# Kernel optimization log

Measured on AMD Instinct MI355X. Metric: run time of the kernel, lower is better.

Reference implementation:

```python
import jax, jax.numpy as jnp
import numpy as np

ROUTING_ITER = 3
EPS = 1e-8


def squash(caps, axis=-1, eps=EPS):
    dot = jnp.sum(caps * caps, axis=axis, keepdims=True)
    scale = dot / (1.0 + dot) / jnp.sqrt(dot + eps)
    return scale * caps


def setup_inputs() -> dict:
    key = jax.random.key(0)
    k1, k2, k3 = jax.random.split(key, 3)
    B, I, O, D_in, D_out = 32, 1024, 64, 16, 32
    x = jax.random.normal(k1, (B, I, D_in), dtype=jnp.float32)
    W = jax.random.normal(k2, (1, I, O, D_out, D_in), dtype=jnp.float32) * 0.05
    b = jax.random.normal(k3, (1, 1, O, D_out), dtype=jnp.float32) * 0.05
    return {"x": x, "W": W, "b": b}


def reference(x, W, b):
    # u_hat[b,i,o,d] = sum_n W[0,i,o,d,n] * x[b,i,n]
    u_hat = jnp.einsum('iodn,bin->biod', W[0], x)  # [B, I, O, D_out]
    u_hat_det = jax.lax.stop_gradient(u_hat)
    B, I, O, _ = u_hat.shape
    b_ij = jnp.zeros((B, I, O, 1), dtype=x.dtype)
    v_j = None
    for it in range(ROUTING_ITER):
        c_ij = jax.nn.softmax(b_ij, axis=2)  # over output capsules
        if it == ROUTING_ITER - 1:
            s_j = jnp.sum(c_ij * u_hat, axis=1, keepdims=True) + b  # [B,1,O,D]
            v_j = squash(s_j, axis=-1)
        else:
            s_j = jnp.sum(c_ij * u_hat_det, axis=1, keepdims=True)
            v_j = squash(s_j, axis=-1)
            a_ij = jnp.sum(u_hat_det * v_j, axis=-1, keepdims=True)  # agreement
            b_ij = b_ij + a_ij
    return jnp.squeeze(v_j)  # [B, O, D_out]
```

## Files before the change

kernel.cpp:

```cpp
#include <hip/hip_runtime.h>
#include <hip/hip_bf16.h>
#include <stdint.h>

#define B_  32
#define I_  1024
#define O_  64
#define D_  32
#define N_  16
#define OD_ 2048

__device__ __forceinline__ uint32_t f2bf1(float f) {
  uint32_t u = __float_as_uint(f);
  return (u + 0x7fffu + ((u >> 16) & 1u)) >> 16;
}
__device__ __forceinline__ uint32_t pack2(float a, float b) {
  return f2bf1(a) | (f2bf1(b) << 16);
}
__device__ __forceinline__ void unpack8(uint4 r, float u[8]) {
  u[0] = __uint_as_float(r.x << 16);
  u[1] = __uint_as_float(r.x & 0xffff0000u);
  u[2] = __uint_as_float(r.y << 16);
  u[3] = __uint_as_float(r.y & 0xffff0000u);
  u[4] = __uint_as_float(r.z << 16);
  u[5] = __uint_as_float(r.z & 0xffff0000u);
  u[6] = __uint_as_float(r.w << 16);
  u[7] = __uint_as_float(r.w & 0xffff0000u);
}

__global__ __launch_bounds__(256) void k_einsum(const float* __restrict__ x,
                                                const float* __restrict__ W,
                                                uint4* __restrict__ uhat) {
  const int i = blockIdx.x;
  const int t = threadIdx.x;
  __shared__ float xs[B_ * N_];
  for (int e = t; e < B_ * N_; e += 256) {
    int bb = e >> 4, n = e & 15;
    xs[e] = x[(size_t)bb * (I_ * N_) + (size_t)i * N_ + n];
  }
  float w[8][16];
  const float* Wi = W + (size_t)i * (OD_ * N_) + (size_t)t * (8 * N_);
  #pragma unroll
  for (int k = 0; k < 8; ++k) {
    #pragma unroll
    for (int q = 0; q < 4; ++q) {
      float4 f = ((const float4*)(Wi + k * 16))[q];
      w[k][q * 4 + 0] = f.x; w[k][q * 4 + 1] = f.y;
      w[k][q * 4 + 2] = f.z; w[k][q * 4 + 3] = f.w;
    }
  }
  __syncthreads();
  for (int bb = 0; bb < B_; ++bb) {
    float xv[16];
    #pragma unroll
    for (int q = 0; q < 4; ++q) {
      float4 f = ((const float4*)(xs + bb * 16))[q];
      xv[q * 4 + 0] = f.x; xv[q * 4 + 1] = f.y;
      xv[q * 4 + 2] = f.z; xv[q * 4 + 3] = f.w;
    }
    float acc[8];
    #pragma unroll
    for (int k = 0; k < 8; ++k) {
      float a = 0.f;
      #pragma unroll
      for (int n = 0; n < 16; ++n) a = fmaf(w[k][n], xv[n], a);
      acc[k] = a;
    }
    uint4 outv = make_uint4(pack2(acc[0], acc[1]), pack2(acc[2], acc[3]),
                            pack2(acc[4], acc[5]), pack2(acc[6], acc[7]));
    uhat[(((size_t)bb * I_ + i) * OD_ + (size_t)t * 8) >> 3] = outv;
  }
}

__global__ __launch_bounds__(256) void k_sum0(const uint4* __restrict__ uhat,
                                              float* __restrict__ part) {
  const int b = blockIdx.x >> 5, chunk = blockIdx.x & 31;
  const int t = threadIdx.x;
  float acc[8] = {0.f, 0.f, 0.f, 0.f, 0.f, 0.f, 0.f, 0.f};
  for (int ii = 0; ii < 32; ++ii) {
    const int i = chunk * 32 + ii;
    uint4 r = uhat[(((size_t)b * I_ + i) * OD_ + (size_t)t * 8) >> 3];
    float u[8]; unpack8(r, u);
    #pragma unroll
    for (int j = 0; j < 8; ++j) acc[j] += u[j];
  }
  float* o = part + ((size_t)b * 32 + chunk) * OD_ + (size_t)t * 8;
  ((float4*)o)[0] = make_float4(acc[0], acc[1], acc[2], acc[3]);
  ((float4*)o)[1] = make_float4(acc[4], acc[5], acc[6], acc[7]);
}

__global__ __launch_bounds__(256) void k_squash(const float* __restrict__ part,
                                                const float* __restrict__ bias,
                                                float* __restrict__ vout,
                                                float scale, int addBias) {
  const int lane = threadIdx.x & 63;
  const int row = blockIdx.x * 4 + (threadIdx.x >> 6);
  const int b = row >> 6, o = row & 63;
  const int d = lane & 31;
  const float* p = part + (size_t)b * (32 * OD_) + (size_t)o * 32 + d;
  float s = 0.f;
  const int c0 = (lane >> 5) * 16;
  for (int c = c0; c < c0 + 16; ++c) s += p[(size_t)c * OD_];
  s += __shfl_xor(s, 32);
  s *= scale;
  if (addBias) s += bias[o * 32 + d];
  float dot = s * s;
  #pragma unroll
  for (int off = 1; off <= 16; off <<= 1) dot += __shfl_xor(dot, off);
  float sc = dot / (1.f + dot) / sqrtf(dot + 1e-8f);
  if (lane < 32) vout[(size_t)row * 32 + d] = s * sc;
}

__global__ __launch_bounds__(256) void k_route(const uint4* __restrict__ uhat,
                                               const float* __restrict__ vprev,
                                               float* __restrict__ bij,
                                               float* __restrict__ part,
                                               int secondIter) {
  const int b = blockIdx.x >> 5, chunk = blockIdx.x & 31;
  const int t = threadIdx.x;
  __shared__ float abuf[64];
  __shared__ float cbuf[64];
  float vreg[8];
  {
    const float4* vp = (const float4*)(vprev + (size_t)b * OD_ + (size_t)t * 8);
    float4 v0 = vp[0], v1 = vp[1];
    vreg[0] = v0.x; vreg[1] = v0.y; vreg[2] = v0.z; vreg[3] = v0.w;
    vreg[4] = v1.x; vreg[5] = v1.y; vreg[6] = v1.z; vreg[7] = v1.w;
  }
  float s_acc[8] = {0.f, 0.f, 0.f, 0.f, 0.f, 0.f, 0.f, 0.f};
  for (int ii = 0; ii < 32; ++ii) {
    const int i = chunk * 32 + ii;
    uint4 r = uhat[(((size_t)b * I_ + i) * OD_ + (size_t)t * 8) >> 3];
    float u[8]; unpack8(r, u);
    float p = 0.f;
    #pragma unroll
    for (int j = 0; j < 8; ++j) p = fmaf(u[j], vreg[j], p);
    p += __shfl_xor(p, 1);
    p += __shfl_xor(p, 2);
    if ((t & 3) == 0) abuf[t >> 2] = p;
    __syncthreads();
    if (t < 64) {
      float a = abuf[t];
      const size_t bidx = ((size_t)b * I_ + i) * 64 + t;
      float bn;
      if (secondIter) bn = bij[bidx] + a;
      else            { bn = a; bij[bidx] = bn; }
      float m = bn;
      #pragma unroll
      for (int off = 1; off <= 32; off <<= 1) m = fmaxf(m, __shfl_xor(m, off));
      float e = __expf(bn - m);
      float sm = e;
      #pragma unroll
      for (int off = 1; off <= 32; off <<= 1) sm += __shfl_xor(sm, off);
      cbuf[t] = e / sm;
    }
    __syncthreads();
    const float c = cbuf[t >> 2];
    #pragma unroll
    for (int j = 0; j < 8; ++j) s_acc[j] = fmaf(c, u[j], s_acc[j]);
  }
  float* o = part + ((size_t)b * 32 + chunk) * OD_ + (size_t)t * 8;
  ((float4*)o)[0] = make_float4(s_acc[0], s_acc[1], s_acc[2], s_acc[3]);
  ((float4*)o)[1] = make_float4(s_acc[4], s_acc[5], s_acc[6], s_acc[7]);
}

extern "C" void kernel_launch(void* const* d_in, const int* in_sizes, int n_in,
                              void* d_out, int out_size, void* d_ws, size_t ws_size,
                              hipStream_t stream) {
  const float* x    = (const float*)d_in[0];
  const float* W    = (const float*)d_in[1];
  const float* bias = (const float*)d_in[2];
  float* out = (float*)d_out;

  char* ws = (char*)d_ws;
  uint4* uhat = (uint4*)ws;
  float* bij  = (float*)(ws + 134217728ull);
  float* part = (float*)(ws + 134217728ull + 8388608ull);
  float* vbuf = (float*)(ws + 134217728ull + 16777216ull);

  k_einsum<<<dim3(I_), dim3(256), 0, stream>>>(x, W, uhat);
  k_sum0  <<<dim3(1024), dim3(256), 0, stream>>>(uhat, part);
  k_squash<<<dim3(512),  dim3(256), 0, stream>>>(part, bias, vbuf, 1.f / 64.f, 0);
  k_route <<<dim3(1024), dim3(256), 0, stream>>>(uhat, vbuf, bij, part, 0);
  k_squash<<<dim3(512),  dim3(256), 0, stream>>>(part, bias, vbuf, 1.f, 0);
  k_route <<<dim3(1024), dim3(256), 0, stream>>>(uhat, vbuf, bij, part, 1);
  k_squash<<<dim3(512),  dim3(256), 0, stream>>>(part, bias, out, 1.f, 1);
}
```

Before: 346.1 us.

## Split einsum per quarter, batch routing softmax over 16 inputs, store partials in bf16

```diff
diff --git a/kernel.cpp b/kernel.cpp
--- a/kernel.cpp
+++ b/kernel.cpp
@@ -27,68 +27,67 @@
   u[7] = __uint_as_float(r.w & 0xffff0000u);
 }
 
-__global__ __launch_bounds__(256) void k_einsum(const float* __restrict__ x,
-                                                const float* __restrict__ W,
-                                                uint4* __restrict__ uhat) {
-  const int i = blockIdx.x;
+__global__ __launch_bounds__(256, 8) void k_einsum(const float* __restrict__ x,
+                                                   const float* __restrict__ W,
+                                                   uint32_t* __restrict__ uhat) {
+  const int i = blockIdx.x >> 2;
+  const int q = blockIdx.x & 3;
   const int t = threadIdx.x;
+  const int od_base = q * 512 + t * 2;
   __shared__ float xs[B_ * N_];
   for (int e = t; e < B_ * N_; e += 256) {
     int bb = e >> 4, n = e & 15;
     xs[e] = x[(size_t)bb * (I_ * N_) + (size_t)i * N_ + n];
   }
-  float w[8][16];
-  const float* Wi = W + (size_t)i * (OD_ * N_) + (size_t)t * (8 * N_);
-  #pragma unroll
-  for (int k = 0; k < 8; ++k) {
-    #pragma unroll
-    for (int q = 0; q < 4; ++q) {
-      float4 f = ((const float4*)(Wi + k * 16))[q];
-      w[k][q * 4 + 0] = f.x; w[k][q * 4 + 1] = f.y;
-      w[k][q * 4 + 2] = f.z; w[k][q * 4 + 3] = f.w;
+  float w[2][16];
+  const float* Wi = W + (size_t)i * (OD_ * N_) + (size_t)od_base * N_;
+  #pragma unroll
+  for (int k = 0; k < 2; ++k) {
+    #pragma unroll
+    for (int qq = 0; qq < 4; ++qq) {
+      float4 f = ((const float4*)(Wi + k * 16))[qq];
+      w[k][qq * 4 + 0] = f.x; w[k][qq * 4 + 1] = f.y;
+      w[k][qq * 4 + 2] = f.z; w[k][qq * 4 + 3] = f.w;
     }
   }
   __syncthreads();
+  #pragma unroll 4
   for (int bb = 0; bb < B_; ++bb) {
-    float xv[16];
-    #pragma unroll
-    for (int q = 0; q < 4; ++q) {
-      float4 f = ((const float4*)(xs + bb * 16))[q];
-      xv[q * 4 + 0] = f.x; xv[q * 4 + 1] = f.y;
-      xv[q * 4 + 2] = f.z; xv[q * 4 + 3] = f.w;
+    float4 x0 = ((const float4*)(xs + bb * 16))[0];
+    float4 x1 = ((const float4*)(xs + bb * 16))[1];
+    float4 x2 = ((const float4*)(xs + bb * 16))[2];
+    float4 x3 = ((const float4*)(xs + bb * 16))[3];
+    float xv[16] = {x0.x, x0.y, x0.z, x0.w, x1.x, x1.y, x1.z, x1.w,
+                    x2.x, x2.y, x2.z, x2.w, x3.x, x3.y, x3.z, x3.w};
+    float a0 = 0.f, a1 = 0.f;
+    #pragma unroll
+    for (int n = 0; n < 16; ++n) {
+      a0 = fmaf(w[0][n], xv[n], a0);
+      a1 = fmaf(w[1][n], xv[n], a1);
     }
-    float acc[8];
-    #pragma unroll
-    for (int k = 0; k < 8; ++k) {
-      float a = 0.f;
-      #pragma unroll
-      for (int n = 0; n < 16; ++n) a = fmaf(w[k][n], xv[n], a);
-      acc[k] = a;
-    }
-    uint4 outv = make_uint4(pack2(acc[0], acc[1]), pack2(acc[2], acc[3]),
-                            pack2(acc[4], acc[5]), pack2(acc[6], acc[7]));
-    uhat[(((size_t)bb * I_ + i) * OD_ + (size_t)t * 8) >> 3] = outv;
+    uhat[(((size_t)bb * I_ + i) * OD_ + od_base) >> 1] = pack2(a0, a1);
   }
 }
 
 __global__ __launch_bounds__(256) void k_sum0(const uint4* __restrict__ uhat,
-                                              float* __restrict__ part) {
-  const int b = blockIdx.x >> 5, chunk = blockIdx.x & 31;
+                                              uint4* __restrict__ part) {
+  const int b = blockIdx.x >> 6, chunk = blockIdx.x & 63;
   const int t = threadIdx.x;
   float acc[8] = {0.f, 0.f, 0.f, 0.f, 0.f, 0.f, 0.f, 0.f};
-  for (int ii = 0; ii < 32; ++ii) {
-    const int i = chunk * 32 + ii;
-    uint4 r = uhat[(((size_t)b * I_ + i) * OD_ + (size_t)t * 8) >> 3];
+  const size_t ubase = (((size_t)b * I_ + (size_t)chunk * 16) * OD_ + (size_t)t * 8) >> 3;
+  #pragma unroll 4
+  for (int ii = 0; ii < 16; ++ii) {
+    uint4 r = uhat[ubase + (size_t)ii * (OD_ / 8)];
     float u[8]; unpack8(r, u);
     #pragma unroll
     for (int j = 0; j < 8; ++j) acc[j] += u[j];
   }
-  float* o = part + ((size_t)b * 32 + chunk) * OD_ + (size_t)t * 8;
-  ((float4*)o)[0] = make_float4(acc[0], acc[1], acc[2], acc[3]);
-  ((float4*)o)[1] = make_float4(acc[4], acc[5], acc[6], acc[7]);
-}
-
-__global__ __launch_bounds__(256) void k_squash(const float* __restrict__ part,
+  part[(((size_t)b * 64 + chunk) * OD_ + (size_t)t * 8) >> 3] =
+      make_uint4(pack2(acc[0], acc[1]), pack2(acc[2], acc[3]),
+                 pack2(acc[4], acc[5]), pack2(acc[6], acc[7]));
+}
+
+__global__ __launch_bounds__(256) void k_squash(const uint16_t* __restrict__ part,
                                                 const float* __restrict__ bias,
                                                 float* __restrict__ vout,
                                                 float scale, int addBias) {
@@ -96,10 +95,11 @@
   const int row = blockIdx.x * 4 + (threadIdx.x >> 6);
   const int b = row >> 6, o = row & 63;
   const int d = lane & 31;
-  const float* p = part + (size_t)b * (32 * OD_) + (size_t)o * 32 + d;
+  const uint16_t* p = part + (size_t)b * (64 * OD_) + (size_t)o * 32 + d;
   float s = 0.f;
-  const int c0 = (lane >> 5) * 16;
-  for (int c = c0; c < c0 + 16; ++c) s += p[(size_t)c * OD_];
+  const int c0 = (lane >> 5) * 32;
+  for (int c = c0; c < c0 + 32; ++c)
+    s += __uint_as_float(((uint32_t)p[(size_t)c * OD_]) << 16);
   s += __shfl_xor(s, 32);
   s *= scale;
   if (addBias) s += bias[o * 32 + d];
@@ -110,15 +110,14 @@
   if (lane < 32) vout[(size_t)row * 32 + d] = s * sc;
 }
 
-__global__ __launch_bounds__(256) void k_route(const uint4* __restrict__ uhat,
-                                               const float* __restrict__ vprev,
-                                               float* __restrict__ bij,
-                                               float* __restrict__ part,
-                                               int secondIter) {
-  const int b = blockIdx.x >> 5, chunk = blockIdx.x & 31;
+__global__ __launch_bounds__(256, 4) void k_route(const uint4* __restrict__ uhat,
+                                                  const float* __restrict__ vprev,
+                                                  float* __restrict__ bij,
+                                                  uint4* __restrict__ part,
+                                                  int secondIter) {
+  const int b = blockIdx.x >> 6, chunk = blockIdx.x & 63;
   const int t = threadIdx.x;
-  __shared__ float abuf[64];
-  __shared__ float cbuf[64];
+  __shared__ float abuf[16 * 64];
   float vreg[8];
   {
     const float4* vp = (const float4*)(vprev + (size_t)b * OD_ + (size_t)t * 8);
@@ -126,41 +125,66 @@
     vreg[0] = v0.x; vreg[1] = v0.y; vreg[2] = v0.z; vreg[3] = v0.w;
     vreg[4] = v1.x; vreg[5] = v1.y; vreg[6] = v1.z; vreg[7] = v1.w;
   }
-  float s_acc[8] = {0.f, 0.f, 0.f, 0.f, 0.f, 0.f, 0.f, 0.f};
-  for (int ii = 0; ii < 32; ++ii) {
-    const int i = chunk * 32 + ii;
-    uint4 r = uhat[(((size_t)b * I_ + i) * OD_ + (size_t)t * 8) >> 3];
-    float u[8]; unpack8(r, u);
+  const size_t ubase = (((size_t)b * I_ + (size_t)chunk * 16) * OD_ + (size_t)t * 8) >> 3;
+  uint4 u4[16];
+  #pragma unroll
+  for (int ii = 0; ii < 16; ++ii) {
+    u4[ii] = uhat[ubase + (size_t)ii * (OD_ / 8)];
+    float u[8]; unpack8(u4[ii], u);
     float p = 0.f;
     #pragma unroll
     for (int j = 0; j < 8; ++j) p = fmaf(u[j], vreg[j], p);
     p += __shfl_xor(p, 1);
     p += __shfl_xor(p, 2);
-    if ((t & 3) == 0) abuf[t >> 2] = p;
-    __syncthreads();
-    if (t < 64) {
-      float a = abuf[t];
-      const size_t bidx = ((size_t)b * I_ + i) * 64 + t;
-      float bn;
-      if (secondIter) bn = bij[bidx] + a;
-      else            { bn = a; bij[bidx] = bn; }
-      float m = bn;
+    if ((t & 3) == 0) abuf[ii * 64 + (t >> 2)] = p;
+  }
+  __syncthreads();
+  {
+    const int ii = t >> 4;
+    const int g = t & 15;
+    const int i = chunk * 16 + ii;
+    float bn[4];
+    const size_t bidx = ((size_t)b * I_ + i) * 64 + g * 4;
+    if (secondIter) {
+      float4 b0 = *((const float4*)(bij + bidx));
+      bn[0] = b0.x + abuf[ii * 64 + g * 4 + 0];
+      bn[1] = b0.y + abuf[ii * 64 + g * 4 + 1];
+      bn[2] = b0.z + abuf[ii * 64 + g * 4 + 2];
+      bn[3] = b0.w + abuf[ii * 64 + g * 4 + 3];
+    } else {
       #pragma unroll
-      for (int off = 1; off <= 32; off <<= 1) m = fmaxf(m, __shfl_xor(m, off));
-      float e = __expf(bn - m);
-      float sm = e;
-      #pragma unroll
-      for (int off = 1; off <= 32; off <<= 1) sm += __shfl_xor(sm, off);
-      cbuf[t] = e / sm;
+      for (int j = 0; j < 4; ++j) bn[j] = abuf[ii * 64 + g * 4 + j];
+      *((float4*)(bij + bidx)) = make_float4(bn[0], bn[1], bn[2], bn[3]);
     }
-    __syncthreads();
-    const float c = cbuf[t >> 2];
+    float m = fmaxf(fmaxf(bn[0], bn[1]), fmaxf(bn[2], bn[3]));
+    m = fmaxf(m, __shfl_xor(m, 1));
+    m = fmaxf(m, __shfl_xor(m, 2));
+    m = fmaxf(m, __shfl_xor(m, 4));
+    m = fmaxf(m, __shfl_xor(m, 8));
+    float e[4], sm = 0.f;
+    #pragma unroll
+    for (int j = 0; j < 4; ++j) { e[j] = __expf(bn[j] - m); sm += e[j]; }
+    sm += __shfl_xor(sm, 1);
+    sm += __shfl_xor(sm, 2);
+    sm += __shfl_xor(sm, 4);
+    sm += __shfl_xor(sm, 8);
+    float inv = 1.f / sm;
+    #pragma unroll
+    for (int j = 0; j < 4; ++j) abuf[ii * 64 + g * 4 + j] = e[j] * inv;
+  }
+  __syncthreads();
+  float s_acc[8] = {0.f, 0.f, 0.f, 0.f, 0.f, 0.f, 0.f, 0.f};
+  const int oq = t >> 2;
+  #pragma unroll
+  for (int ii = 0; ii < 16; ++ii) {
+    float u[8]; unpack8(u4[ii], u);
+    const float c = abuf[ii * 64 + oq];
     #pragma unroll
     for (int j = 0; j < 8; ++j) s_acc[j] = fmaf(c, u[j], s_acc[j]);
   }
-  float* o = part + ((size_t)b * 32 + chunk) * OD_ + (size_t)t * 8;
-  ((float4*)o)[0] = make_float4(s_acc[0], s_acc[1], s_acc[2], s_acc[3]);
-  ((float4*)o)[1] = make_float4(s_acc[4], s_acc[5], s_acc[6], s_acc[7]);
+  part[(((size_t)b * 64 + chunk) * OD_ + (size_t)t * 8) >> 3] =
+      make_uint4(pack2(s_acc[0], s_acc[1]), pack2(s_acc[2], s_acc[3]),
+                 pack2(s_acc[4], s_acc[5]), pack2(s_acc[6], s_acc[7]));
 }
 
 extern "C" void kernel_launch(void* const* d_in, const int* in_sizes, int n_in,
@@ -172,16 +196,18 @@
   float* out = (float*)d_out;
 
   char* ws = (char*)d_ws;
-  uint4* uhat = (uint4*)ws;
+  uint32_t* uhat1 = (uint32_t*)ws;
+  uint4*    uhat4 = (uint4*)ws;
   float* bij  = (float*)(ws + 134217728ull);
-  float* part = (float*)(ws + 134217728ull + 8388608ull);
+  uint4* part = (uint4*)(ws + 134217728ull + 8388608ull);
+  uint16_t* part16 = (uint16_t*)part;
   float* vbuf = (float*)(ws + 134217728ull + 16777216ull);
 
-  k_einsum<<<dim3(I_), dim3(256), 0, stream>>>(x, W, uhat);
-  k_sum0  <<<dim3(1024), dim3(256), 0, stream>>>(uhat, part);
-  k_squash<<<dim3(512),  dim3(256), 0, stream>>>(part, bias, vbuf, 1.f / 64.f, 0);
-  k_route <<<dim3(1024), dim3(256), 0, stream>>>(uhat, vbuf, bij, part, 0);
-  k_squash<<<dim3(512),  dim3(256), 0, stream>>>(part, bias, vbuf, 1.f, 0);
-  k_route <<<dim3(1024), dim3(256), 0, stream>>>(uhat, vbuf, bij, part, 1);
-  k_squash<<<dim3(512),  dim3(256), 0, stream>>>(part, bias, out, 1.f, 1);
-}
+  k_einsum<<<dim3(I_ * 4), dim3(256), 0, stream>>>(x, W, uhat1);
+  k_sum0  <<<dim3(2048), dim3(256), 0, stream>>>(uhat4, part);
+  k_squash<<<dim3(512),  dim3(256), 0, stream>>>(part16, bias, vbuf, 1.f / 64.f, 0);
+  k_route <<<dim3(2048), dim3(256), 0, stream>>>(uhat4, vbuf, bij, part, 0);
+  k_squash<<<dim3(512),  dim3(256), 0, stream>>>(part16, bias, vbuf, 1.f, 0);
+  k_route <<<dim3(2048), dim3(256), 0, stream>>>(uhat4, vbuf, bij, part, 1);
+  k_squash<<<dim3(512),  dim3(256), 0, stream>>>(part16, bias, out, 1.f, 1);
+}
```

Result: slower. 820.6 us (+137.1%).
